# Kernel optimization log

Measured on AMD Instinct MI355X. Metric: run time of the kernel, lower is better.

The kernel has to match this reference:

```python
import jax, jax.numpy as jnp
import numpy as np

B, S, D = 2, 2048, 2048
H, KVH, HD = 32, 8, 64
GROUPS = H // KVH  # 4
NEG = -1e9


def setup_inputs() -> dict:
    key = jax.random.key(0)
    ks = jax.random.split(key, 5)
    x = jax.random.normal(ks[0], (B, S, D), dtype=jnp.float32)
    # causal additive mask [1,1,S,S]
    causal = jnp.triu(jnp.full((S, S), NEG, dtype=jnp.float32), k=1)[None, None]
    Wq = jax.random.normal(ks[1], (D, D), dtype=jnp.float32) * (D ** -0.5)
    Wk = jax.random.normal(ks[2], (KVH * HD, D), dtype=jnp.float32) * (D ** -0.5)
    Wv = jax.random.normal(ks[3], (KVH * HD, D), dtype=jnp.float32) * (D ** -0.5)
    Wo = jax.random.normal(ks[4], (D, D), dtype=jnp.float32) * (D ** -0.5)
    return {"x": x, "attention_mask": causal, "Wq": Wq, "Wk": Wk, "Wv": Wv, "Wo": Wo}


def reference(x, attention_mask, Wq, Wk, Wv, Wo):
    b, s, _ = x.shape
    # projections (nn.Linear: y = x @ W.T)
    q = (x @ Wq.T).reshape(b, s, H, HD).transpose(0, 2, 1, 3)      # [b,H,s,hd]
    k = (x @ Wk.T).reshape(b, s, KVH, HD).transpose(0, 2, 1, 3)    # [b,KVH,s,hd]
    v = (x @ Wv.T).reshape(b, s, KVH, HD).transpose(0, 2, 1, 3)
    new_kv_cache = (k, v)
    # repeat_interleave over head dim for GQA
    k = jnp.repeat(k, GROUPS, axis=1)  # [b,H,s,hd]
    v = jnp.repeat(v, GROUPS, axis=1)
    scale = 1.0 / jnp.sqrt(jnp.float32(HD))
    scores = jnp.einsum('bhqd,bhkd->bhqk', q, k) * scale
    scores = scores + attention_mask
    attn = jax.nn.softmax(scores.astype(jnp.float32), axis=-1).astype(q.dtype)
    out = jnp.einsum('bhqk,bhkd->bhqd', attn, v)  # [b,H,s,hd]
    out = out.transpose(0, 2, 1, 3).reshape(b, s, H * HD)
    output = out @ Wo.T
    return (output, new_kv_cache[0], new_kv_cache[1])
```

## Files before the change

### kernel.cpp

```cpp
#include <hip/hip_runtime.h>
#include <hip/hip_bf16.h>
#include <stdint.h>

#define B_ 2
#define S_ 2048
#define D_ 2048
#define H_ 32
#define KVH_ 8
#define HD_ 64

typedef __bf16 bf16x8 __attribute__((ext_vector_type(8)));
typedef float f32x4 __attribute__((ext_vector_type(4)));

#define MFMA16(a, b, c) __builtin_amdgcn_mfma_f32_16x16x32_bf16((a), (b), (c), 0, 0, 0)

typedef __attribute__((address_space(1))) void gvoid_t;
typedef __attribute__((address_space(3))) void lvoid_t;

__device__ __forceinline__ void async_ld16(__hip_bfloat16* lds, const __hip_bfloat16* g) {
  __builtin_amdgcn_global_load_lds((gvoid_t*)(void*)(g), (lvoid_t*)(lds), 16, 0, 0);
}

__device__ __forceinline__ unsigned short f2bu(float f) {
  __hip_bfloat16 h = __float2bfloat16(f);
  return *reinterpret_cast<unsigned short*>(&h);
}

__global__ void cast_bf16_kernel(const float* __restrict__ in,
                                 unsigned short* __restrict__ out, int n4) {
  int i = blockIdx.x * blockDim.x + threadIdx.x;
  if (i >= n4) return;
  float4 v = reinterpret_cast<const float4*>(in)[i];
  ushort4 o;
  o.x = f2bu(v.x); o.y = f2bu(v.y); o.z = f2bu(v.z); o.w = f2bu(v.w);
  reinterpret_cast<ushort4*>(out)[i] = o;
}

template <int MODE>
__global__ __launch_bounds__(256, 2)
void gemm_bt(const __hip_bfloat16* __restrict__ A,
             const __hip_bfloat16* __restrict__ W,
             float* __restrict__ Cf, __hip_bfloat16* __restrict__ Cb,
             float* __restrict__ Cf2, __hip_bfloat16* __restrict__ Cb2,
             __hip_bfloat16* __restrict__ Cb3,
             int M, int N, int K) {
  __shared__ __align__(16) __hip_bfloat16 sA[128 * 32];
  __shared__ __align__(16) __hip_bfloat16 sB[128 * 32];
  const int tid = threadIdx.x;
  const int lane = tid & 63;
  const int wv = tid >> 6;
  const int l15 = lane & 15, l4 = lane >> 4;
  const int bm = blockIdx.x * 128, bn = blockIdx.y * 128;
  const int wm = (wv >> 1) * 64, wn = (wv & 1) * 64;

  const int ci0 = tid, ci1 = tid + 256;
  const __hip_bfloat16* gA0 = A + (size_t)(bm + (ci0 >> 2)) * K + (ci0 & 3) * 8;
  const __hip_bfloat16* gA1 = A + (size_t)(bm + (ci1 >> 2)) * K + (ci1 & 3) * 8;
  const __hip_bfloat16* gB0 = W + (size_t)(bn + (ci0 >> 2)) * K + (ci0 & 3) * 8;
  const __hip_bfloat16* gB1 = W + (size_t)(bn + (ci1 >> 2)) * K + (ci1 & 3) * 8;
  __hip_bfloat16* lA0 = &sA[ci0 * 8];
  __hip_bfloat16* lA1 = &sA[ci1 * 8];
  __hip_bfloat16* lB0 = &sB[ci0 * 8];
  __hip_bfloat16* lB1 = &sB[ci1 * 8];

  f32x4 acc[4][4];
#pragma unroll
  for (int i = 0; i < 4; ++i) {
#pragma unroll
    for (int j = 0; j < 4; ++j) acc[i][j] = f32x4{0.f, 0.f, 0.f, 0.f};
  }

  for (int k0 = 0; k0 < K; k0 += 32) {
    async_ld16(lA0, gA0 + k0);
    async_ld16(lA1, gA1 + k0);
    async_ld16(lB0, gB0 + k0);
    async_ld16(lB1, gB1 + k0);
    __syncthreads();
    bf16x8 af[4], bfr[4];
#pragma unroll
    for (int i = 0; i < 4; ++i)
      af[i] = *reinterpret_cast<const bf16x8*>(&sA[(wm + i * 16 + l15) * 32 + l4 * 8]);
#pragma unroll
    for (int j = 0; j < 4; ++j)
      bfr[j] = *reinterpret_cast<const bf16x8*>(&sB[(wn + j * 16 + l15) * 32 + l4 * 8]);
#pragma unroll
    for (int i = 0; i < 4; ++i) {
#pragma unroll
      for (int j = 0; j < 4; ++j) acc[i][j] = MFMA16(af[i], bfr[j], acc[i][j]);
    }
    __syncthreads();
  }

#pragma unroll
  for (int i = 0; i < 4; ++i) {
#pragma unroll
    for (int j = 0; j < 4; ++j) {
      const int col = bn + wn + j * 16 + l15;
#pragma unroll
      for (int r = 0; r < 4; ++r) {
        const int row = bm + wm + i * 16 + l4 * 4 + r;
        const float v = acc[i][j][r];
        if (MODE == 1) {
          Cf[(size_t)row * N + col] = v;
        } else {
          if (bn < 2048) {
            Cb[(size_t)row * 2048 + col] = __float2bfloat16(v);
          } else {
            const int bb = row >> 11, s = row & 2047;
            const int kv = col - 2048;
            if (kv < 512) {
              const int g = kv >> 6, hd = kv & 63;
              const size_t idx = ((size_t)(bb * KVH_ + g) * S_ + s) * HD_ + hd;
              Cf[idx] = v;
              Cb2[idx] = __float2bfloat16(v);
            } else {
              const int vv = kv - 512;
              const int g = vv >> 6, hd = vv & 63;
              const size_t idx = ((size_t)(bb * KVH_ + g) * S_ + s) * HD_ + hd;
              Cf2[idx] = v;
              Cb3[((size_t)(bb * KVH_ + g) * HD_ + hd) * S_ + s] = __float2bfloat16(v);
            }
          }
        }
      }
    }
  }
}

__global__ __launch_bounds__(256, 2)
void attn_fused(const __hip_bfloat16* __restrict__ Qb,
                const __hip_bfloat16* __restrict__ Kb,
                const __hip_bfloat16* __restrict__ Vtb,
                __hip_bfloat16* __restrict__ AOb) {
  constexpr int SKS = 72;
  constexpr int SVS = 136;
  constexpr int SPS = 64;
  __shared__ __align__(16) __hip_bfloat16 sK[128 * SKS];
  __shared__ __align__(16) __hip_bfloat16 sV[64 * SVS];
  __shared__ __align__(16) __hip_bfloat16 sP[4 * 32 * SPS];

  const int tid = threadIdx.x;
  const int lane = tid & 63;
  const int wv = tid >> 6;
  const int l15 = lane & 15, l4 = lane >> 4;
  const int qa = blockIdx.x;
  const int qb = 15 - qa;
  const int h = blockIdx.y;
  const int b = blockIdx.z;
  const int g = h >> 2;

  bf16x8 qfA[2][2], qfB[2][2];
  {
    const __hip_bfloat16* QpA =
        Qb + ((size_t)(b * S_ + qa * 128 + wv * 32)) * D_ + h * HD_;
    const __hip_bfloat16* QpB =
        Qb + ((size_t)(b * S_ + qb * 128 + wv * 32)) * D_ + h * HD_;
#pragma unroll
    for (int i = 0; i < 2; ++i) {
#pragma unroll
      for (int c = 0; c < 2; ++c) {
        qfA[i][c] = *reinterpret_cast<const bf16x8*>(
            QpA + (size_t)(i * 16 + l15) * D_ + c * 32 + l4 * 8);
        qfB[i][c] = *reinterpret_cast<const bf16x8*>(
            QpB + (size_t)(i * 16 + l15) * D_ + c * 32 + l4 * 8);
      }
    }
  }

  float mstA[2][4], mstB[2][4];
  f32x4 oaccA[2][4], oaccB[2][4];
  f32x4 laccA[2], laccB[2];
#pragma unroll
  for (int i = 0; i < 2; ++i) {
#pragma unroll
    for (int r = 0; r < 4; ++r) { mstA[i][r] = -3.0e38f; mstB[i][r] = -3.0e38f; }
    laccA[i] = f32x4{0.f, 0.f, 0.f, 0.f};
    laccB[i] = f32x4{0.f, 0.f, 0.f, 0.f};
#pragma unroll
    for (int j = 0; j < 4; ++j) {
      oaccA[i][j] = f32x4{0.f, 0.f, 0.f, 0.f};
      oaccB[i][j] = f32x4{0.f, 0.f, 0.f, 0.f};
    }
  }

  bf16x8 vone;
#pragma unroll
  for (int j = 0; j < 8; ++j) vone[j] = (__bf16)1.0f;

  const __hip_bfloat16* Kp = Kb + (size_t)(b * KVH_ + g) * S_ * HD_;
  const __hip_bfloat16* Vp = Vtb + (size_t)(b * KVH_ + g) * HD_ * S_;
  __hip_bfloat16* sPw = sP + wv * 32 * SPS;
  const float CE = 0.125f * 1.4426950408889634f;

  auto process = [&](bf16x8 (&qf)[2][2], float (&mst)[2][4], f32x4 (&lacc)[2],
                     f32x4 (&oacc)[2][4], bool diag) {
    f32x4 sc[2][8];
#pragma unroll
    for (int jn = 0; jn < 8; ++jn) {
      const bf16x8 k0 = *reinterpret_cast<const bf16x8*>(&sK[(jn * 16 + l15) * SKS + l4 * 8]);
      const bf16x8 k1 = *reinterpret_cast<const bf16x8*>(&sK[(jn * 16 + l15) * SKS + 32 + l4 * 8]);
#pragma unroll
      for (int i = 0; i < 2; ++i) {
        f32x4 t = f32x4{0.f, 0.f, 0.f, 0.f};
        t = MFMA16(qf[i][0], k0, t);
        t = MFMA16(qf[i][1], k1, t);
        sc[i][jn] = t;
      }
    }

    if (diag) {
#pragma unroll
      for (int i = 0; i < 2; ++i) {
#pragma unroll
        for (int jn = 0; jn < 8; ++jn) {
          const int kp = jn * 16 + l15;
#pragma unroll
          for (int r = 0; r < 4; ++r) {
            const int qp = wv * 32 + i * 16 + l4 * 4 + r;
            if (kp > qp) sc[i][jn][r] = -3.0e38f;
          }
        }
      }
    }

    float alph[2][4];
#pragma unroll
    for (int i = 0; i < 2; ++i) {
#pragma unroll
      for (int r = 0; r < 4; ++r) {
        float mx = sc[i][0][r];
#pragma unroll
        for (int jn = 1; jn < 8; ++jn) mx = fmaxf(mx, sc[i][jn][r]);
#pragma unroll
        for (int off = 1; off < 16; off <<= 1) mx = fmaxf(mx, __shfl_xor(mx, off, 64));
        const float Mn = fmaxf(mst[i][r], mx * CE);
        alph[i][r] = exp2f(mst[i][r] - Mn);
        mst[i][r] = Mn;
#pragma unroll
        for (int jn = 0; jn < 8; ++jn)
          sc[i][jn][r] = exp2f(fmaf(sc[i][jn][r], CE, -Mn));
      }
    }
#pragma unroll
    for (int i = 0; i < 2; ++i) {
#pragma unroll
      for (int r = 0; r < 4; ++r) lacc[i][r] *= alph[i][r];
#pragma unroll
      for (int j = 0; j < 4; ++j) {
#pragma unroll
        for (int r = 0; r < 4; ++r) oacc[i][j][r] *= alph[i][r];
      }
    }

#pragma unroll
    for (int hh = 0; hh < 2; ++hh) {
#pragma unroll
      for (int i = 0; i < 2; ++i) {
#pragma unroll
        for (int jj = 0; jj < 4; ++jj) {
#pragma unroll
          for (int r = 0; r < 4; ++r)
            sPw[(i * 16 + l4 * 4 + r) * SPS + ((jj ^ l4) * 16 + l15)] =
                __float2bfloat16(sc[i][hh * 4 + jj][r]);
        }
      }
      const int gr = (l15 >> 2) & 3;
#pragma unroll
      for (int kc = 0; kc < 2; ++kc) {
        bf16x8 vf[4];
#pragma unroll
        for (int jn = 0; jn < 4; ++jn)
          vf[jn] = *reinterpret_cast<const bf16x8*>(
              &sV[(jn * 16 + l15) * SVS + hh * 64 + kc * 32 + l4 * 8]);
#pragma unroll
        for (int i = 0; i < 2; ++i) {
          const bf16x8 pf = *reinterpret_cast<const bf16x8*>(
              &sPw[(i * 16 + l15) * SPS + (((kc * 2 + (l4 >> 1)) ^ gr) * 16 + (l4 & 1) * 8)]);
#pragma unroll
          for (int jn = 0; jn < 4; ++jn) oacc[i][jn] = MFMA16(pf, vf[jn], oacc[i][jn]);
          lacc[i] = MFMA16(pf, vone, lacc[i]);
        }
      }
    }
  };

  bf16x8 kreg[4], vreg[4];
  auto load_tile = [&](int ki) {
#pragma unroll
    for (int t = 0; t < 4; ++t) {
      const int ci = tid + t * 256;
      kreg[t] = *reinterpret_cast<const bf16x8*>(
          Kp + (size_t)(ki * 128 + (ci >> 3)) * HD_ + (ci & 7) * 8);
    }
#pragma unroll
    for (int t = 0; t < 4; ++t) {
      const int ci = tid + t * 256;
      vreg[t] = *reinterpret_cast<const bf16x8*>(
          Vp + (size_t)(ci >> 4) * S_ + ki * 128 + (ci & 15) * 8);
    }
  };

  load_tile(0);
  for (int ki = 0; ki <= qb; ++ki) {
#pragma unroll
    for (int t = 0; t < 4; ++t) {
      const int ci = tid + t * 256;
      *reinterpret_cast<bf16x8*>(&sK[(ci >> 3) * SKS + (ci & 7) * 8]) = kreg[t];
    }
#pragma unroll
    for (int t = 0; t < 4; ++t) {
      const int ci = tid + t * 256;
      *reinterpret_cast<bf16x8*>(&sV[(ci >> 4) * SVS + (ci & 15) * 8]) = vreg[t];
    }
    __syncthreads();
    if (ki < qb) load_tile(ki + 1);

    process(qfB, mstB, laccB, oaccB, ki == qb);
    if (ki <= qa) process(qfA, mstA, laccA, oaccA, ki == qa);
    __syncthreads();
  }

#pragma unroll
  for (int tsel = 0; tsel < 2; ++tsel) {
    const int qt = tsel ? qb : qa;
    f32x4 (&oacc)[2][4] = tsel ? oaccB : oaccA;
    f32x4 (&lacc)[2] = tsel ? laccB : laccA;
#pragma unroll
    for (int i = 0; i < 2; ++i) {
      float inv[4];
#pragma unroll
      for (int r = 0; r < 4; ++r) inv[r] = 1.0f / lacc[i][r];
#pragma unroll
      for (int jn = 0; jn < 4; ++jn) {
#pragma unroll
        for (int r = 0; r < 4; ++r) {
          const int qp = qt * 128 + wv * 32 + i * 16 + l4 * 4 + r;
          AOb[(size_t)(b * S_ + qp) * D_ + h * HD_ + jn * 16 + l15] =
              __float2bfloat16(oacc[i][jn][r] * inv[r]);
        }
      }
    }
  }
}

extern "C" void kernel_launch(void* const* d_in, const int* in_sizes, int n_in,
                              void* d_out, int out_size, void* d_ws, size_t ws_size,
                              hipStream_t stream) {
  (void)in_sizes; (void)n_in; (void)out_size; (void)ws_size;
  const float* x = (const float*)d_in[0];
  const float* Wq = (const float*)d_in[2];
  const float* Wk = (const float*)d_in[3];
  const float* Wv = (const float*)d_in[4];
  const float* Wo = (const float*)d_in[5];

  float* outO = (float*)d_out;
  float* outK = outO + (size_t)B_ * S_ * D_;
  float* outV = outK + (size_t)B_ * KVH_ * S_ * HD_;

  char* p = (char*)d_ws;
  __hip_bfloat16* xb    = (__hip_bfloat16*)p; p += (size_t)B_ * S_ * D_ * 2;
  __hip_bfloat16* Wqkvb = (__hip_bfloat16*)p; p += (size_t)3072 * D_ * 2;
  __hip_bfloat16* Wob   = (__hip_bfloat16*)p; p += (size_t)D_ * D_ * 2;
  __hip_bfloat16* Qbf   = (__hip_bfloat16*)p; p += (size_t)B_ * S_ * D_ * 2;
  __hip_bfloat16* Kbf   = (__hip_bfloat16*)p; p += (size_t)B_ * KVH_ * S_ * HD_ * 2;
  __hip_bfloat16* Vtb   = (__hip_bfloat16*)p; p += (size_t)B_ * KVH_ * S_ * HD_ * 2;
  __hip_bfloat16* AOb   = (__hip_bfloat16*)p; p += (size_t)B_ * S_ * D_ * 2;

  auto cast = [&](const float* src, __hip_bfloat16* dst, size_t n) {
    const int n4 = (int)(n / 4);
    cast_bf16_kernel<<<dim3((n4 + 255) / 256), dim3(256), 0, stream>>>(
        src, (unsigned short*)dst, n4);
  };
  cast(x, xb, (size_t)B_ * S_ * D_);
  cast(Wq, Wqkvb, (size_t)D_ * D_);
  cast(Wk, Wqkvb + (size_t)2048 * D_, (size_t)KVH_ * HD_ * D_);
  cast(Wv, Wqkvb + (size_t)2560 * D_, (size_t)KVH_ * HD_ * D_);
  cast(Wo, Wob, (size_t)D_ * D_);

  gemm_bt<4><<<dim3(32, 24), dim3(256), 0, stream>>>(
      xb, Wqkvb, outK, Qbf, outV, Kbf, Vtb, 4096, 3072, 2048);
  attn_fused<<<dim3(8, 32, 2), dim3(256), 0, stream>>>(Qbf, Kbf, Vtb, AOb);
  gemm_bt<1><<<dim3(32, 16), dim3(256), 0, stream>>>(
      AOb, Wob, outO, nullptr, nullptr, nullptr, nullptr, 4096, 2048, 2048);
}
```

Before: 373.6 us.

## Double-buffer 64-key K/V tiles in LDS with async global-to-LDS loads

Replaces the register-staged 128-key K/V tiles with two 64-key LDS buffers filled by direct global-to-LDS async loads, so the next tile's fetch overlaps the current tile's compute. The loop needs only one barrier per step instead of two. Row padding is dropped in favour of an XOR swizzle to avoid bank conflicts. The causal mask logic is adapted to half-tile offsets. In exchange there are twice as many loop iterations, with more softmax rescale work per key. Correctness also depends on the async loads being complete before the barrier.

After: 377.0 us. Within noise of the previous version (+0.9%).

```diff
diff --git a/kernel.cpp b/kernel.cpp
--- a/kernel.cpp
+++ b/kernel.cpp
@@ -132,11 +132,9 @@
                 const __hip_bfloat16* __restrict__ Kb,
                 const __hip_bfloat16* __restrict__ Vtb,
                 __hip_bfloat16* __restrict__ AOb) {
-  constexpr int SKS = 72;
-  constexpr int SVS = 136;
+  __shared__ __align__(16) __hip_bfloat16 sK[2][64 * 64];
+  __shared__ __align__(16) __hip_bfloat16 sV[2][64 * 64];
   constexpr int SPS = 64;
-  __shared__ __align__(16) __hip_bfloat16 sK[128 * SKS];
-  __shared__ __align__(16) __hip_bfloat16 sV[64 * SVS];
   __shared__ __align__(16) __hip_bfloat16 sP[4 * 32 * SPS];
 
   const int tid = threadIdx.x;
@@ -192,13 +190,33 @@
   __hip_bfloat16* sPw = sP + wv * 32 * SPS;
   const float CE = 0.125f * 1.4426950408889634f;
 
-  auto process = [&](bf16x8 (&qf)[2][2], float (&mst)[2][4], f32x4 (&lacc)[2],
-                     f32x4 (&oacc)[2][4], bool diag) {
-    f32x4 sc[2][8];
-#pragma unroll
-    for (int jn = 0; jn < 8; ++jn) {
-      const bf16x8 k0 = *reinterpret_cast<const bf16x8*>(&sK[(jn * 16 + l15) * SKS + l4 * 8]);
-      const bf16x8 k1 = *reinterpret_cast<const bf16x8*>(&sK[(jn * 16 + l15) * SKS + 32 + l4 * 8]);
+  auto stage = [&](int kt, int buf) {
+#pragma unroll
+    for (int t = 0; t < 2; ++t) {
+      const int p = tid + t * 256;
+      const int r = p >> 3, cp = p & 7;
+      const int c = cp ^ (r & 7);
+      async_ld16(&sK[buf][p * 8], Kp + (size_t)(kt * 64 + r) * HD_ + c * 8);
+    }
+#pragma unroll
+    for (int t = 0; t < 2; ++t) {
+      const int p = tid + t * 256;
+      const int r = p >> 3, cp = p & 7;
+      const int c = cp ^ (r & 7);
+      async_ld16(&sV[buf][p * 8], Vp + (size_t)r * S_ + kt * 64 + c * 8);
+    }
+  };
+
+  auto process = [&](int buf, int koff, bf16x8 (&qf)[2][2], float (&mst)[2][4],
+                     f32x4 (&lacc)[2], f32x4 (&oacc)[2][4]) {
+    f32x4 sc[2][4];
+#pragma unroll
+    for (int jn = 0; jn < 4; ++jn) {
+      const int row = jn * 16 + l15;
+      const bf16x8 k0 = *reinterpret_cast<const bf16x8*>(
+          &sK[buf][(row * 8 + (l4 ^ (row & 7))) * 8]);
+      const bf16x8 k1 = *reinterpret_cast<const bf16x8*>(
+          &sK[buf][(row * 8 + ((4 + l4) ^ (row & 7))) * 8]);
 #pragma unroll
       for (int i = 0; i < 2; ++i) {
         f32x4 t = f32x4{0.f, 0.f, 0.f, 0.f};
@@ -208,12 +226,12 @@
       }
     }
 
-    if (diag) {
+    if (koff >= 0) {
 #pragma unroll
       for (int i = 0; i < 2; ++i) {
 #pragma unroll
-        for (int jn = 0; jn < 8; ++jn) {
-          const int kp = jn * 16 + l15;
+        for (int jn = 0; jn < 4; ++jn) {
+          const int kp = koff + jn * 16 + l15;
 #pragma unroll
           for (int r = 0; r < 4; ++r) {
             const int qp = wv * 32 + i * 16 + l4 * 4 + r;
@@ -230,14 +248,14 @@
       for (int r = 0; r < 4; ++r) {
         float mx = sc[i][0][r];
 #pragma unroll
-        for (int jn = 1; jn < 8; ++jn) mx = fmaxf(mx, sc[i][jn][r]);
+        for (int jn = 1; jn < 4; ++jn) mx = fmaxf(mx, sc[i][jn][r]);
 #pragma unroll
         for (int off = 1; off < 16; off <<= 1) mx = fmaxf(mx, __shfl_xor(mx, off, 64));
         const float Mn = fmaxf(mst[i][r], mx * CE);
         alph[i][r] = exp2f(mst[i][r] - Mn);
         mst[i][r] = Mn;
 #pragma unroll
-        for (int jn = 0; jn < 8; ++jn)
+        for (int jn = 0; jn < 4; ++jn)
           sc[i][jn][r] = exp2f(fmaf(sc[i][jn][r], CE, -Mn));
       }
     }
@@ -253,71 +271,46 @@
     }
 
 #pragma unroll
-    for (int hh = 0; hh < 2; ++hh) {
+    for (int i = 0; i < 2; ++i) {
+#pragma unroll
+      for (int jj = 0; jj < 4; ++jj) {
+#pragma unroll
+        for (int r = 0; r < 4; ++r)
+          sPw[(i * 16 + l4 * 4 + r) * SPS + ((jj ^ l4) * 16 + l15)] =
+              __float2bfloat16(sc[i][jj][r]);
+      }
+    }
+    const int gr = (l15 >> 2) & 3;
+#pragma unroll
+    for (int kc = 0; kc < 2; ++kc) {
+      bf16x8 vf[4];
+#pragma unroll
+      for (int jn = 0; jn < 4; ++jn) {
+        const int row = jn * 16 + l15;
+        vf[jn] = *reinterpret_cast<const bf16x8*>(
+            &sV[buf][(row * 8 + ((kc * 4 + l4) ^ (row & 7))) * 8]);
+      }
 #pragma unroll
       for (int i = 0; i < 2; ++i) {
-#pragma unroll
-        for (int jj = 0; jj < 4; ++jj) {
-#pragma unroll
-          for (int r = 0; r < 4; ++r)
-            sPw[(i * 16 + l4 * 4 + r) * SPS + ((jj ^ l4) * 16 + l15)] =
-                __float2bfloat16(sc[i][hh * 4 + jj][r]);
-        }
-      }
-      const int gr = (l15 >> 2) & 3;
-#pragma unroll
-      for (int kc = 0; kc < 2; ++kc) {
-        bf16x8 vf[4];
-#pragma unroll
-        for (int jn = 0; jn < 4; ++jn)
-          vf[jn] = *reinterpret_cast<const bf16x8*>(
-              &sV[(jn * 16 + l15) * SVS + hh * 64 + kc * 32 + l4 * 8]);
-#pragma unroll
-        for (int i = 0; i < 2; ++i) {
-          const bf16x8 pf = *reinterpret_cast<const bf16x8*>(
-              &sPw[(i * 16 + l15) * SPS + (((kc * 2 + (l4 >> 1)) ^ gr) * 16 + (l4 & 1) * 8)]);
-#pragma unroll
-          for (int jn = 0; jn < 4; ++jn) oacc[i][jn] = MFMA16(pf, vf[jn], oacc[i][jn]);
-          lacc[i] = MFMA16(pf, vone, lacc[i]);
-        }
+        const bf16x8 pf = *reinterpret_cast<const bf16x8*>(
+            &sPw[(i * 16 + l15) * SPS + (((kc * 2 + (l4 >> 1)) ^ gr) * 16 + (l4 & 1) * 8)]);
+#pragma unroll
+        for (int jn = 0; jn < 4; ++jn) oacc[i][jn] = MFMA16(pf, vf[jn], oacc[i][jn]);
+        lacc[i] = MFMA16(pf, vone, lacc[i]);
       }
     }
   };
 
-  bf16x8 kreg[4], vreg[4];
-  auto load_tile = [&](int ki) {
-#pragma unroll
-    for (int t = 0; t < 4; ++t) {
-      const int ci = tid + t * 256;
-      kreg[t] = *reinterpret_cast<const bf16x8*>(
-          Kp + (size_t)(ki * 128 + (ci >> 3)) * HD_ + (ci & 7) * 8);
-    }
-#pragma unroll
-    for (int t = 0; t < 4; ++t) {
-      const int ci = tid + t * 256;
-      vreg[t] = *reinterpret_cast<const bf16x8*>(
-          Vp + (size_t)(ci >> 4) * S_ + ki * 128 + (ci & 15) * 8);
-    }
-  };
-
-  load_tile(0);
-  for (int ki = 0; ki <= qb; ++ki) {
-#pragma unroll
-    for (int t = 0; t < 4; ++t) {
-      const int ci = tid + t * 256;
-      *reinterpret_cast<bf16x8*>(&sK[(ci >> 3) * SKS + (ci & 7) * 8]) = kreg[t];
-    }
-#pragma unroll
-    for (int t = 0; t < 4; ++t) {
-      const int ci = tid + t * 256;
-      *reinterpret_cast<bf16x8*>(&sV[(ci >> 4) * SVS + (ci & 15) * 8]) = vreg[t];
-    }
+  const int nsteps = 2 * qb + 2;
+  const int kiA_max = 2 * qa + 1;
+  stage(0, 0);
+  for (int ki = 0; ki < nsteps; ++ki) {
+    const int cur = ki & 1;
     __syncthreads();
-    if (ki < qb) load_tile(ki + 1);
-
-    process(qfB, mstB, laccB, oaccB, ki == qb);
-    if (ki <= qa) process(qfA, mstA, laccA, oaccA, ki == qa);
-    __syncthreads();
+    if (ki + 1 < nsteps) stage(ki + 1, cur ^ 1);
+    process(cur, ((ki >> 1) == qb) ? ((ki & 1) * 64) : -1, qfB, mstB, laccB, oaccB);
+    if (ki <= kiA_max)
+      process(cur, ((ki >> 1) == qa) ? ((ki & 1) * 64) : -1, qfA, mstA, laccA, oaccA);
   }
 
 #pragma unroll
```
